# Performance work log

Measured on AMD Instinct MI355X. Metric: run time of the kernel, lower is better.

## Reference

```python
import jax, jax.numpy as jnp
import numpy as np

B, T, D = 64, 512, 512   # batch, time, input features
L, H = 3, 512            # num stacked LSTM layers, hidden size


def setup_inputs() -> dict:
    key = jax.random.key(0)
    kx, kw, ku, kb = jax.random.split(key, 4)
    x = jax.random.normal(kx, (B, T, D), dtype=jnp.float32)
    # Kernel [in, 4H], recurrent kernel [H, 4H], bias [4H] per layer, stacked.
    # Scale weights down to avoid immediate gate saturation.
    W = jax.random.normal(kw, (L, D, 4 * H), dtype=jnp.float32) * 0.05
    U = jax.random.normal(ku, (L, H, 4 * H), dtype=jnp.float32) * 0.05
    b = jax.random.normal(kb, (L, 4 * H), dtype=jnp.float32) * 0.05
    return {"x": x, "W": W, "U": U, "b": b}


def reference(x, W, U, b):
    """Stacked LSTM (Keras LSTMCell math, gate order i,f,g,o), return final top h."""
    nL = W.shape[0]
    nB = x.shape[0]
    nH = U.shape[1]

    def step(carry, xt):
        h, c = carry  # each [L, B, H]
        inp = xt      # [B, D]
        new_h, new_c = [], []
        for l in range(nL):
            z = inp @ W[l] + h[l] @ U[l] + b[l]           # [B, 4H]
            i, f, g, o = jnp.split(z, 4, axis=-1)
            i = jax.nn.sigmoid(i)
            f = jax.nn.sigmoid(f)
            g = jnp.tanh(g)
            o = jax.nn.sigmoid(o)
            cn = f * c[l] + i * g
            hn = o * jnp.tanh(cn)
            new_h.append(hn)
            new_c.append(cn)
            inp = hn
        return (jnp.stack(new_h), jnp.stack(new_c)), None

    h0 = jnp.zeros((nL, nB, nH), x.dtype)
    c0 = jnp.zeros((nL, nB, nH), x.dtype)
    xt = jnp.swapaxes(x, 0, 1)  # [T, B, D]
    (hT, cT), _ = jax.lax.scan(step, (h0, c0), xt)
    return hT[-1]  # [B, H] final hidden state of top layer (return_sequences=False)
```

## Files before the change

kernel.cpp:

```cpp
#include <hip/hip_runtime.h>
#include <math.h>


#define T_ 512
#define RING_US (3 * 8 * 64 * 512)
#define XH_OFF_US (2 * 1024 * 1024)
#define XL_OFF_US (XH_OFF_US + 16777216)
#define WS_NEED_XS ((size_t)(XL_OFF_US + 16777216) * 2)

typedef float f32x4 __attribute__((ext_vector_type(4)));
typedef short s16x8 __attribute__((ext_vector_type(8)));

__device__ __forceinline__ unsigned short bf16hi(float f) {
  unsigned u = __float_as_uint(f);
  u += 0x7FFFu + ((u >> 16) & 1u);
  return (unsigned short)(u >> 16);
}
__device__ __forceinline__ float bf2f(unsigned short h) {
  return __uint_as_float(((unsigned)h) << 16);
}
__device__ __forceinline__ float sigf(float z) { return 1.f / (1.f + __expf(-z)); }
__device__ __forceinline__ float tanhf_(float z) { return 2.f * sigf(2.f * z) - 1.f; }

__device__ __forceinline__ void split8(const float* p, s16x8* hi, s16x8* lo) {
  union { s16x8 s; unsigned u[4]; } Uh, Ul;
#pragma unroll
  for (int e = 0; e < 4; ++e) {
    float f0 = p[2 * e], f1 = p[2 * e + 1];
    unsigned short h0 = bf16hi(f0), h1 = bf16hi(f1);
    unsigned short l0 = bf16hi(f0 - bf2f(h0)), l1 = bf16hi(f1 - bf2f(h1));
    Uh.u[e] = (unsigned)h0 | ((unsigned)h1 << 16);
    Ul.u[e] = (unsigned)l0 | ((unsigned)l1 << 16);
  }
  *hi = Uh.s; *lo = Ul.s;
}

__device__ __forceinline__ void do_mfma(const s16x8* ah, const s16x8* al,
                                        s16x8 bh0, s16x8 bh1, s16x8 bl0, s16x8 bl1,
                                        f32x4 acc[4][2]) {
#pragma unroll
  for (int m = 0; m < 4; ++m) {
    acc[m][0] = __builtin_amdgcn_mfma_f32_16x16x32_bf16(ah[m], bh0, acc[m][0], 0, 0, 0);
    acc[m][0] = __builtin_amdgcn_mfma_f32_16x16x32_bf16(ah[m], bl0, acc[m][0], 0, 0, 0);
    acc[m][0] = __builtin_amdgcn_mfma_f32_16x16x32_bf16(al[m], bh0, acc[m][0], 0, 0, 0);
    acc[m][1] = __builtin_amdgcn_mfma_f32_16x16x32_bf16(ah[m], bh1, acc[m][1], 0, 0, 0);
    acc[m][1] = __builtin_amdgcn_mfma_f32_16x16x32_bf16(ah[m], bl1, acc[m][1], 0, 0, 0);
    acc[m][1] = __builtin_amdgcn_mfma_f32_16x16x32_bf16(al[m], bh1, acc[m][1], 0, 0, 0);
  }
}

__global__ __launch_bounds__(256) void init_kernel(const float* __restrict__ x,
                                                   float* __restrict__ ws_f,
                                                   int do_x) {
  unsigned short* rh = (unsigned short*)ws_f;
  unsigned short* rl = rh + RING_US;
  unsigned int* done = (unsigned int*)(rh + 2 * RING_US);
  const int bid = blockIdx.x, tid = threadIdx.x;
  if (bid < 2048) {
    if (!do_x) return;
    __shared__ float tile[64 * 132];
    const int t = bid >> 2, dq = bid & 3;
#pragma unroll
    for (int i = 0; i < 32; ++i) {
      int idx = tid + i * 256;
      int b = idx >> 7, dd = idx & 127;
      tile[b * 132 + dd] = x[((size_t)b * 512 + t) * 512 + dq * 128 + dd];
    }
    __syncthreads();
    ushort4* xh4 = (ushort4*)(rh + XH_OFF_US);
    ushort4* xl4 = (ushort4*)(rh + XL_OFF_US);
#pragma unroll
    for (int i = 0; i < 8; ++i) {
      int o4 = tid + i * 256;
      int dl = o4 >> 7;
      int b = (o4 >> 1) & 63;
      int c4 = (o4 & 1) * 4;
      const float* tp = tile + b * 132 + dl * 8 + c4;
      float f0 = tp[0], f1 = tp[1], f2 = tp[2], f3 = tp[3];
      unsigned short h0 = bf16hi(f0), h1 = bf16hi(f1), h2 = bf16hi(f2), h3 = bf16hi(f3);
      ushort4 vh = make_ushort4(h0, h1, h2, h3);
      ushort4 vl = make_ushort4(bf16hi(f0 - bf2f(h0)), bf16hi(f1 - bf2f(h1)),
                                bf16hi(f2 - bf2f(h2)), bf16hi(f3 - bf2f(h3)));
      int gi = t * 8192 + (dq * 16 + dl) * 128 + b * 2 + (o4 & 1);
      xh4[gi] = vh;
      xl4[gi] = vl;
    }
  } else {
    const int idx0 = (bid - 2048) * 256 + tid;
    for (int e = idx0; e < 3 * 32768; e += 8 * 256) {
      int l = e >> 15, off = e & 32767;
      rh[l * 262144 + off] = 0;
      rl[l * 262144 + off] = 0;
    }
    for (int e = idx0; e < 3 * T_; e += 8 * 256) done[e] = 0u;
  }
}

template <bool XS>
__global__ __launch_bounds__(256) void lstm_kernel(const float* __restrict__ W,
                                                   const float* __restrict__ U,
                                                   const float* __restrict__ bia,
                                                   const float* __restrict__ x,
                                                   float* __restrict__ ws_f,
                                                   float* __restrict__ out) {
  __shared__ unsigned short smWh[32 * 1032];
  __shared__ float pbuf[8192];

  const int tid = threadIdx.x;
  const int l = blockIdx.x >> 6;
  const int cg = blockIdx.x & 63;
  const int w = tid >> 6;
  const int lane = tid & 63;
  const int cl = lane & 15, kg = lane >> 4;
  const int j = lane & 7, rp = lane >> 3;

  unsigned short* rh = (unsigned short*)ws_f;
  unsigned short* rl = rh + RING_US;
  unsigned int* done = (unsigned int*)(rh + 2 * RING_US);

  {
    unsigned short* plo = (unsigned short*)pbuf;
    const int c = tid & 31, ks0 = tid >> 5;
    const int gcol = (c >> 3) * 512 + cg * 8 + (c & 7);
    for (int k = ks0; k < 1024; k += 8) {
      float f = (k < 512) ? W[((size_t)l * 512 + k) * 2048 + gcol]
                          : U[((size_t)l * 512 + (k - 512)) * 2048 + gcol];
      unsigned short h = bf16hi(f);
      smWh[c * 1032 + (k >> 3) * 8 + (k & 7)] = h;
      if (k < 512) plo[c * 512 + k] = bf16hi(f - bf2f(h));
    }
  }
  __syncthreads();
  s16x8 wl[2][8];
  if (w < 2) {
#pragma unroll
    for (int nt = 0; nt < 2; ++nt)
#pragma unroll
      for (int ks = 0; ks < 8; ++ks)
        wl[nt][ks] = *(const s16x8*)((const unsigned short*)pbuf +
                       (nt * 16 + cl) * 512 + w * 256 + ks * 32 + kg * 8);
  }
  __syncthreads();
  {
    unsigned short* plo = (unsigned short*)pbuf;
    const int c = tid & 31, ks0 = tid >> 5;
    const int gcol = (c >> 3) * 512 + cg * 8 + (c & 7);
    for (int k = 512 + ks0; k < 1024; k += 8) {
      float f = U[((size_t)l * 512 + (k - 512)) * 2048 + gcol];
      unsigned short h = bf16hi(f);
      plo[c * 512 + (k - 512)] = bf16hi(f - bf2f(h));
    }
  }
  __syncthreads();
  if (w >= 2) {
#pragma unroll
    for (int nt = 0; nt < 2; ++nt)
#pragma unroll
      for (int ks = 0; ks < 8; ++ks)
        wl[nt][ks] = *(const s16x8*)((const unsigned short*)pbuf +
                       (nt * 16 + cl) * 512 + (w - 2) * 256 + ks * 32 + kg * 8);
  }
  __syncthreads();

  const float bias_g[4] = {bia[l * 2048 + 0 * 512 + cg * 8 + j],
                           bia[l * 2048 + 1 * 512 + cg * 8 + j],
                           bia[l * 2048 + 2 * 512 + cg * 8 + j],
                           bia[l * 2048 + 3 * 512 + cg * 8 + j]};
  float c_st0 = 0.f, c_st1 = 0.f;

  const int whb0 = cl * 1032 + w * 256 + kg * 8;
  const int whb1 = (16 + cl) * 1032 + w * 256 + kg * 8;

  for (int t = 0; t < T_; ++t) {
    if (tid == 0) {
      if (l > 0)
        while (__hip_atomic_load(&done[(l - 1) * T_ + t], __ATOMIC_RELAXED,
                                 __HIP_MEMORY_SCOPE_AGENT) < 64u)
          __builtin_amdgcn_s_sleep(1);
      if (t > 0)
        while (__hip_atomic_load(&done[l * T_ + t - 1], __ATOMIC_RELAXED,
                                 __HIP_MEMORY_SCOPE_AGENT) < 64u)
          __builtin_amdgcn_s_sleep(1);
      if (t >= 8) {
        while (__hip_atomic_load(&done[l * T_ + t - 7], __ATOMIC_RELAXED,
                                 __HIP_MEMORY_SCOPE_AGENT) < 64u)
          __builtin_amdgcn_s_sleep(1);
        if (l < 2)
          while (__hip_atomic_load(&done[(l + 1) * T_ + t - 8], __ATOMIC_RELAXED,
                                   __HIP_MEMORY_SCOPE_AGENT) < 64u)
            __builtin_amdgcn_s_sleep(1);
      }
      __builtin_amdgcn_fence(__ATOMIC_ACQUIRE, "agent");
    }
    __syncthreads();

    const int slot = (t + 1) & 7, pslot = t & 7;
    f32x4 acc[4][2];
#pragma unroll
    for (int m = 0; m < 4; ++m) { acc[m][0] = (f32x4)(0.f); acc[m][1] = (f32x4)(0.f); }

    if (!XS && l == 0 && w < 2) {
      for (int ks = 0; ks < 8; ++ks) {
        s16x8 ah[4], al[4];
#pragma unroll
        for (int m = 0; m < 4; ++m)
          split8(x + ((size_t)(m * 16 + cl) * 512 + t) * 512 + w * 256 + ks * 32 + kg * 8,
                 &ah[m], &al[m]);
        s16x8 bh0 = *(const s16x8*)(smWh + whb0 + ks * 32);
        s16x8 bh1 = *(const s16x8*)(smWh + whb1 + ks * 32);
        do_mfma(ah, al, bh0, bh1, wl[0][ks], wl[1][ks], acc);
      }
    } else {
      const unsigned short *pah, *pal;
      int cb;
      if (w < 2) {
        if (XS && l == 0) {
          pah = rh + XH_OFF_US + t * 32768;
          pal = rh + XL_OFF_US + t * 32768;
        } else {
          pah = rh + ((l - 1) * 8 + slot) * 32768;
          pal = rl + ((l - 1) * 8 + slot) * 32768;
        }
        cb = w * 32;
      } else {
        pah = rh + (l * 8 + pslot) * 32768;
        pal = rl + (l * 8 + pslot) * 32768;
        cb = (w - 2) * 32;
      }
      for (int ks = 0; ks < 8; ++ks) {
        s16x8 ah[4], al[4];
#pragma unroll
        for (int m = 0; m < 4; ++m) {
          int off = (cb + ks * 4 + kg) * 512 + (m * 16 + cl) * 8;
          ah[m] = *(const s16x8*)(pah + off);
          al[m] = *(const s16x8*)(pal + off);
        }
        s16x8 bh0 = *(const s16x8*)(smWh + whb0 + ks * 32);
        s16x8 bh1 = *(const s16x8*)(smWh + whb1 + ks * 32);
        do_mfma(ah, al, bh0, bh1, wl[0][ks], wl[1][ks], acc);
      }
    }

#pragma unroll
    for (int m = 0; m < 4; ++m)
#pragma unroll
      for (int n = 0; n < 2; ++n)
        *(f32x4*)(pbuf + (((w * 4 + m) * 2 + n) * 16 + cl) * 16 + kg * 4) = acc[m][n];
    __syncthreads();

    float z0[4], z1[4];
#pragma unroll
    for (int g = 0; g < 4; ++g) {
      int nt = g >> 1, cc = (g & 1) * 8 + j;
      float a0 = 0.f, a1 = 0.f;
#pragma unroll
      for (int sw = 0; sw < 4; ++sw) {
        float2 v = *(const float2*)(pbuf + (((sw * 4 + w) * 2 + nt) * 16 + cc) * 16 +
                                    (rp >> 1) * 4 + (rp & 1) * 2);
        a0 += v.x; a1 += v.y;
      }
      z0[g] = a0 + bias_g[g]; z1[g] = a1 + bias_g[g];
    }
    float iv0 = sigf(z0[0]), fv0 = sigf(z0[1]), gv0 = tanhf_(z0[2]), ov0 = sigf(z0[3]);
    float iv1 = sigf(z1[0]), fv1 = sigf(z1[1]), gv1 = tanhf_(z1[2]), ov1 = sigf(z1[3]);
    c_st0 = fv0 * c_st0 + iv0 * gv0;
    c_st1 = fv1 * c_st1 + iv1 * gv1;
    float h0 = ov0 * tanhf_(c_st0);
    float h1 = ov1 * tanhf_(c_st1);

    const int grow0 = w * 16 + rp * 2, grow1 = grow0 + 1;
    unsigned short hh0 = bf16hi(h0), hh1 = bf16hi(h1);
    unsigned short hl0 = bf16hi(h0 - bf2f(hh0)), hl1 = bf16hi(h1 - bf2f(hh1));
    size_t wb = (size_t)(l * 8 + slot) * 32768 + cg * 512;
    rh[wb + grow0 * 8 + j] = hh0;
    rl[wb + grow0 * 8 + j] = hl0;
    rh[wb + grow1 * 8 + j] = hh1;
    rl[wb + grow1 * 8 + j] = hl1;
    if (l == 2 && t == T_ - 1) {
      out[grow0 * 512 + cg * 8 + j] = h0;
      out[grow1 * 512 + cg * 8 + j] = h1;
    }
    __syncthreads();

    if (tid == 0) {
      __hip_atomic_fetch_add(&done[l * T_ + t], 1u, __ATOMIC_RELEASE,
                             __HIP_MEMORY_SCOPE_AGENT);
    }
  }
}

extern "C" void kernel_launch(void* const* d_in, const int* in_sizes, int n_in,
                              void* d_out, int out_size, void* d_ws, size_t ws_size,
                              hipStream_t stream) {
  (void)in_sizes; (void)n_in; (void)out_size;
  const float* x = (const float*)d_in[0];
  const float* W = (const float*)d_in[1];
  const float* U = (const float*)d_in[2];
  const float* b = (const float*)d_in[3];
  float* out = (float*)d_out;
  float* ws = (float*)d_ws;
  const int xs = (ws_size >= WS_NEED_XS) ? 1 : 0;

  hipLaunchKernelGGL(init_kernel, dim3(2056), dim3(256), 0, stream, x, ws, xs);
  if (xs)
    hipLaunchKernelGGL((lstm_kernel<true>), dim3(192), dim3(256), 0, stream,
                       W, U, b, x, ws, out);
  else
    hipLaunchKernelGGL((lstm_kernel<false>), dim3(192), dim3(256), 0, stream,
                       W, U, b, x, ws, out);
}
```

Before: 10.05 ms.

## Replace counter barriers with per-block progress flags and per-wave dependency waits

Each block now publishes its completed timestep into its own flag slot with a release store, replacing the per-timestep atomic counter. Waiting is done wave-wide: each lane polls one producer flag and the wave exits once all lanes are satisfied. Waves that consume the layer-below input and waves that consume the recurrent state now wait only on their own dependencies, so the input-side MFMA work can start before the recurrent dependency is ready. This aims to shorten the serial handoff on the critical path, at the cost of more polling traffic and more careful ordering between independent waves.

```diff
diff --git a/kernel.cpp b/kernel.cpp
--- a/kernel.cpp
+++ b/kernel.cpp
@@ -49,12 +49,22 @@
   }
 }
 
+__device__ __forceinline__ void wait_flags(const unsigned int* f, int lane,
+                                           unsigned int tgt) {
+  while (true) {
+    unsigned int v = __hip_atomic_load(&f[lane], __ATOMIC_RELAXED,
+                                       __HIP_MEMORY_SCOPE_AGENT);
+    if (__all((int)(v >= tgt))) break;
+    __builtin_amdgcn_s_sleep(1);
+  }
+}
+
 __global__ __launch_bounds__(256) void init_kernel(const float* __restrict__ x,
                                                    float* __restrict__ ws_f,
                                                    int do_x) {
   unsigned short* rh = (unsigned short*)ws_f;
   unsigned short* rl = rh + RING_US;
-  unsigned int* done = (unsigned int*)(rh + 2 * RING_US);
+  unsigned int* flags = (unsigned int*)(rh + 2 * RING_US);
   const int bid = blockIdx.x, tid = threadIdx.x;
   if (bid < 2048) {
     if (!do_x) return;
@@ -92,7 +102,7 @@
       rh[l * 262144 + off] = 0;
       rl[l * 262144 + off] = 0;
     }
-    for (int e = idx0; e < 3 * T_; e += 8 * 256) done[e] = 0u;
+    if (idx0 < 192) flags[idx0] = 0u;
   }
 }
 
@@ -116,7 +126,7 @@
 
   unsigned short* rh = (unsigned short*)ws_f;
   unsigned short* rl = rh + RING_US;
-  unsigned int* done = (unsigned int*)(rh + 2 * RING_US);
+  unsigned int* flags = (unsigned int*)(rh + 2 * RING_US);
 
   {
     unsigned short* plo = (unsigned short*)pbuf;
@@ -172,48 +182,29 @@
   const int whb1 = (16 + cl) * 1032 + w * 256 + kg * 8;
 
   for (int t = 0; t < T_; ++t) {
-    if (tid == 0) {
-      if (l > 0)
-        while (__hip_atomic_load(&done[(l - 1) * T_ + t], __ATOMIC_RELAXED,
-                                 __HIP_MEMORY_SCOPE_AGENT) < 64u)
-          __builtin_amdgcn_s_sleep(1);
-      if (t > 0)
-        while (__hip_atomic_load(&done[l * T_ + t - 1], __ATOMIC_RELAXED,
-                                 __HIP_MEMORY_SCOPE_AGENT) < 64u)
-          __builtin_amdgcn_s_sleep(1);
-      if (t >= 8) {
-        while (__hip_atomic_load(&done[l * T_ + t - 7], __ATOMIC_RELAXED,
-                                 __HIP_MEMORY_SCOPE_AGENT) < 64u)
-          __builtin_amdgcn_s_sleep(1);
-        if (l < 2)
-          while (__hip_atomic_load(&done[(l + 1) * T_ + t - 8], __ATOMIC_RELAXED,
-                                   __HIP_MEMORY_SCOPE_AGENT) < 64u)
-            __builtin_amdgcn_s_sleep(1);
-      }
-      __builtin_amdgcn_fence(__ATOMIC_ACQUIRE, "agent");
-    }
-    __syncthreads();
-
     const int slot = (t + 1) & 7, pslot = t & 7;
     f32x4 acc[4][2];
 #pragma unroll
     for (int m = 0; m < 4; ++m) { acc[m][0] = (f32x4)(0.f); acc[m][1] = (f32x4)(0.f); }
 
-    if (!XS && l == 0 && w < 2) {
-      for (int ks = 0; ks < 8; ++ks) {
-        s16x8 ah[4], al[4];
-#pragma unroll
-        for (int m = 0; m < 4; ++m)
-          split8(x + ((size_t)(m * 16 + cl) * 512 + t) * 512 + w * 256 + ks * 32 + kg * 8,
-                 &ah[m], &al[m]);
-        s16x8 bh0 = *(const s16x8*)(smWh + whb0 + ks * 32);
-        s16x8 bh1 = *(const s16x8*)(smWh + whb1 + ks * 32);
-        do_mfma(ah, al, bh0, bh1, wl[0][ks], wl[1][ks], acc);
+    if (w < 2) {
+      if (l > 0) {
+        wait_flags(flags + (l - 1) * 64, lane, (unsigned)(t + 1));
+        __builtin_amdgcn_fence(__ATOMIC_ACQUIRE, "agent");
       }
-    } else {
-      const unsigned short *pah, *pal;
-      int cb;
-      if (w < 2) {
+      if (!XS && l == 0) {
+        for (int ks = 0; ks < 8; ++ks) {
+          s16x8 ah[4], al[4];
+#pragma unroll
+          for (int m = 0; m < 4; ++m)
+            split8(x + ((size_t)(m * 16 + cl) * 512 + t) * 512 + w * 256 + ks * 32 + kg * 8,
+                   &ah[m], &al[m]);
+          s16x8 bh0 = *(const s16x8*)(smWh + whb0 + ks * 32);
+          s16x8 bh1 = *(const s16x8*)(smWh + whb1 + ks * 32);
+          do_mfma(ah, al, bh0, bh1, wl[0][ks], wl[1][ks], acc);
+        }
+      } else {
+        const unsigned short *pah, *pal;
         if (XS && l == 0) {
           pah = rh + XH_OFF_US + t * 32768;
           pal = rh + XL_OFF_US + t * 32768;
@@ -221,12 +212,28 @@
           pah = rh + ((l - 1) * 8 + slot) * 32768;
           pal = rl + ((l - 1) * 8 + slot) * 32768;
         }
-        cb = w * 32;
-      } else {
-        pah = rh + (l * 8 + pslot) * 32768;
-        pal = rl + (l * 8 + pslot) * 32768;
-        cb = (w - 2) * 32;
+        const int cb = w * 32;
+        for (int ks = 0; ks < 8; ++ks) {
+          s16x8 ah[4], al[4];
+#pragma unroll
+          for (int m = 0; m < 4; ++m) {
+            int off = (cb + ks * 4 + kg) * 512 + (m * 16 + cl) * 8;
+            ah[m] = *(const s16x8*)(pah + off);
+            al[m] = *(const s16x8*)(pal + off);
+          }
+          s16x8 bh0 = *(const s16x8*)(smWh + whb0 + ks * 32);
+          s16x8 bh1 = *(const s16x8*)(smWh + whb1 + ks * 32);
+          do_mfma(ah, al, bh0, bh1, wl[0][ks], wl[1][ks], acc);
+        }
       }
+    } else {
+      wait_flags(flags + l * 64, lane, (unsigned)t);
+      if (l < 2 && t >= 8)
+        wait_flags(flags + (l + 1) * 64, lane, (unsigned)(t - 7));
+      __builtin_amdgcn_fence(__ATOMIC_ACQUIRE, "agent");
+      const unsigned short* pah = rh + (l * 8 + pslot) * 32768;
+      const unsigned short* pal = rl + (l * 8 + pslot) * 32768;
+      const int cb = (w - 2) * 32;
       for (int ks = 0; ks < 8; ++ks) {
         s16x8 ah[4], al[4];
 #pragma unroll
@@ -283,8 +290,8 @@
     __syncthreads();
 
     if (tid == 0) {
-      __hip_atomic_fetch_add(&done[l * T_ + t], 1u, __ATOMIC_RELEASE,
-                             __HIP_MEMORY_SCOPE_AGENT);
+      __hip_atomic_store(&flags[l * 64 + cg], (unsigned)(t + 1), __ATOMIC_RELEASE,
+                         __HIP_MEMORY_SCOPE_AGENT);
     }
   }
 }
```

After: 10.38 ms. +3.3%, slower.
